# Performance work log

Measured on AMD Instinct MI355X. Metric: run time of the kernel, lower is better.

## Reference

```python
import jax, jax.numpy as jnp
import numpy as np

N = 16384   # flat token count
D = 256     # d_model
M = 64      # median_size (attention in_features / hidden_features)
OUT = 1     # output_size


def setup_inputs() -> dict:
    key = jax.random.key(0)
    ks = jax.random.split(key, 12)
    sD = 1.0 / np.sqrt(D)
    sM = 1.0 / np.sqrt(M)
    rn = lambda k, shape, s: (jax.random.normal(k, shape, jnp.float32) * s)
    return {
        "x":    rn(ks[0], (N, D), 1.0),
        "W1":   rn(ks[1], (D, M), sD), "b1": jnp.zeros((M,), jnp.float32),
        # 3 stacked attention blocks
        "Wq":   rn(ks[2], (3, M, M), sM), "bq": jnp.zeros((3, M), jnp.float32),
        "Wk":   rn(ks[3], (3, M, M), sM), "bk": jnp.zeros((3, M), jnp.float32),
        "Wv":   rn(ks[4], (3, M, M), sM), "bv": jnp.zeros((3, M), jnp.float32),
        "Wf1":  rn(ks[5], (3, M, M), sM), "bf1": jnp.zeros((3, M), jnp.float32),
        "Wf2":  rn(ks[6], (3, M, M), sM), "bf2": jnp.zeros((3, M), jnp.float32),
        "ln_g": jnp.ones((3, M), jnp.float32), "ln_b": jnp.zeros((3, M), jnp.float32),
        "Wout": rn(ks[7], (M, OUT), sM), "bout": jnp.zeros((OUT,), jnp.float32),
    }


def leaky(x, slope):
    return jnp.where(x >= 0, x, slope * x)


def layer_norm(x, g, b, eps=1e-5):
    mu = jnp.mean(x, axis=-1, keepdims=True)
    var = jnp.mean((x - mu) ** 2, axis=-1, keepdims=True)
    return (x - mu) * jax.lax.rsqrt(var + eps) * g + b


def attn_block(x, Wq, bq, Wk, bk, Wv, bv, Wf1, bf1, Wf2, bf2):
    # per-token outer-product attention: attn[n] = softmax(q[n] k[n]^T) over last dim
    q = x @ Wq + bq            # [N, M]
    k = x @ Wk + bk
    v = x @ Wv + bv
    a = jax.nn.softmax(q[:, :, None] * k[:, None, :], axis=-1)   # [N, M, M]
    y = jnp.einsum('nij,nj->ni', a, v) + x                       # residual add (x += x0)
    h = leaky(y @ Wf1 + bf1, 0.01)                               # LeakyReLU(0.01)
    h = h @ Wf2 + bf2
    return h + y                                                 # pred=False residual


def reference(x, W1, b1, Wq, bq, Wk, bk, Wv, bv, Wf1, bf1, Wf2, bf2, ln_g, ln_b, Wout, bout):
    h = x @ W1 + b1                 # Linear_1
    res = leaky(h, 0.1)             # x1 = LeakyReLU(0.1)(h)
    cur = h                         # transformer_1 is applied to pre-activation h
    for t in range(3):
        a = attn_block(cur, Wq[t], bq[t], Wk[t], bk[t], Wv[t], bv[t],
                       Wf1[t], bf1[t], Wf2[t], bf2[t])
        a = layer_norm(a, ln_g[t], ln_b[t])
        res = a + res               # x2 = LN(...) + x1, etc.
        cur = res
    out = leaky(res @ Wout + bout, 0.1).reshape(-1, OUT)
    return (out, out, out, out, out)
```

## Files before the change

kernel.cpp:

```cpp
#include <hip/hip_runtime.h>

#define NTOK 16384
#define TB 16

typedef float f32x4_t __attribute__((ext_vector_type(4)));
typedef short s16x8_t __attribute__((ext_vector_type(8)));

union bfpack { unsigned int u[4]; s16x8_t v; };

__device__ __forceinline__ unsigned int pk2bf(float lo, float hi) {
    unsigned int r;
    asm("v_cvt_pk_bf16_f32 %0, %1, %2" : "=v"(r) : "v"(lo), "v"(hi));
    return r;
}
__device__ __forceinline__ unsigned short f2bf(float f) {
    unsigned int r;
    asm("v_cvt_pk_bf16_f32 %0, %1, %1" : "=v"(r) : "v"(f));
    return (unsigned short)r;
}
__device__ __forceinline__ unsigned short f2bf_host_style(float f) {
    unsigned int x = __float_as_uint(f);
    x += 0x7fffu + ((x >> 16) & 1u);
    return (unsigned short)(x >> 16);
}
__device__ __forceinline__ float fexp2(float x) {
#if __has_builtin(__builtin_amdgcn_exp2f)
    return __builtin_amdgcn_exp2f(x);
#else
    return exp2f(x);
#endif
}
__device__ __forceinline__ float frcp(float x) {
#if __has_builtin(__builtin_amdgcn_rcpf)
    return __builtin_amdgcn_rcpf(x);
#else
    return 1.0f / x;
#endif
}
__device__ __forceinline__ float frsq(float x) {
#if __has_builtin(__builtin_amdgcn_rsqf)
    return __builtin_amdgcn_rsqf(x);
#else
    return rsqrtf(x);
#endif
}

__global__ __launch_bounds__(256)
void prep_kernel(const float* __restrict__ W1,
                 const float* __restrict__ Wq, const float* __restrict__ Wk,
                 const float* __restrict__ Wv, const float* __restrict__ Wf1,
                 const float* __restrict__ Wf2, unsigned short* __restrict__ wsb)
{
    const int i = blockIdx.x * 256 + threadIdx.x;
    if (i < 16384) {
        const int m = i >> 8, k = i & 255;
        wsb[i] = f2bf_host_style(W1[k * 64 + m]);
    } else if (i < 77824) {
        const int u  = i - 16384;
        const int mi = u >> 12;
        const int st = mi / 5, q = mi % 5;
        const int r  = u & 4095;
        const int m  = r >> 6, k = r & 63;
        const float* src = q == 0 ? Wq : q == 1 ? Wk : q == 2 ? Wv : q == 3 ? Wf1 : Wf2;
        wsb[i] = f2bf_host_style(src[st * 4096 + k * 64 + m]);
    }
}

__global__ __launch_bounds__(256, 4)
void tf3_kernel(const float* __restrict__ x,
                const float* __restrict__ b1,
                const float* __restrict__ bq, const float* __restrict__ bk,
                const float* __restrict__ bv,
                const float* __restrict__ bf1, const float* __restrict__ bf2,
                const float* __restrict__ lng, const float* __restrict__ lnb,
                const float* __restrict__ Wout, const float* __restrict__ bout,
                const unsigned short* __restrict__ wsb,
                float* __restrict__ out)
{
    __shared__ __align__(16) unsigned short w3_lds[3 * 4096];
    __shared__ __align__(16) unsigned short a_lds[16 * 64];
    __shared__ __align__(16) float q_lds[16 * 68];
    __shared__ __align__(16) float ky_lds[16 * 68];
    __shared__ __align__(16) float v_lds[16 * 68];

    const int tid = threadIdx.x;
    const int wv  = tid >> 6;
    const int l   = tid & 63;
    const int n0  = blockIdx.x * TB;

    const int lr  = l & 15;
    const int q4  = l >> 4;
    const int c   = wv * 16 + lr;

    const int ge = lr;
    const int tg = wv * 4 + q4;

    float res_reg[4], cur_reg[4];

    auto LOAD2 = [&](int matIdx, s16x8_t& r0, s16x8_t& r1) {
        const char* gb = (const char*)(wsb + 16384 + matIdx * 4096) + wv * 2048 + l * 16;
        r0 = *reinterpret_cast<const s16x8_t*>(gb);
        r1 = *reinterpret_cast<const s16x8_t*>(gb + 1024);
    };
    auto WRITE2 = [&](int slot, s16x8_t r0, s16x8_t r1) {
        #pragma unroll
        for (int p = 0; p < 2; ++p) {
            const int b  = wv * 2048 + p * 1024 + l * 16;
            const int mm = b >> 7;
            const int sw = ((b >> 4) & 7) ^ (mm & 7);
            *reinterpret_cast<s16x8_t*>((char*)w3_lds + slot * 8192 + (b & ~127) + (sw << 4))
                = p ? r1 : r0;
        }
    };
    auto mm16 = [&](s16x8_t af0, s16x8_t af1, const unsigned short* bbase) -> f32x4_t {
        const s16x8_t b0  = *reinterpret_cast<const s16x8_t*>(&bbase[c * 64 + (((0 + q4) ^ (c & 7)) * 8)]);
        const s16x8_t b1f = *reinterpret_cast<const s16x8_t*>(&bbase[c * 64 + (((4 + q4) ^ (c & 7)) * 8)]);
        f32x4_t acc = __builtin_amdgcn_mfma_f32_16x16x32_bf16(af0, b0, (f32x4_t){0.f,0.f,0.f,0.f}, 0, 0, 0);
        acc = __builtin_amdgcn_mfma_f32_16x16x32_bf16(af1, b1f, acc, 0, 0, 0);
        return acc;
    };

    s16x8_t wr0, wr1, wr2, wr3, wr4, wr5;

    LOAD2(0, wr0, wr1); LOAD2(1, wr2, wr3); LOAD2(2, wr4, wr5);

    {
        const int r  = tid & 15;
        const int cb = tid >> 4;
        const float* xp = x + (size_t)(n0 + r) * 256 + cb * 16;
        const float4 u0 = *reinterpret_cast<const float4*>(xp);
        const float4 u1 = *reinterpret_cast<const float4*>(xp + 4);
        const float4 u2 = *reinterpret_cast<const float4*>(xp + 8);
        const float4 u3 = *reinterpret_cast<const float4*>(xp + 12);
        bfpack P0, P1;
        P0.u[0] = pk2bf(u0.x, u0.y); P0.u[1] = pk2bf(u0.z, u0.w);
        P0.u[2] = pk2bf(u1.x, u1.y); P0.u[3] = pk2bf(u1.z, u1.w);
        P1.u[0] = pk2bf(u2.x, u2.y); P1.u[1] = pk2bf(u2.z, u2.w);
        P1.u[2] = pk2bf(u3.x, u3.y); P1.u[3] = pk2bf(u3.z, u3.w);
        char* rowb = (char*)w3_lds + r * 512;
        *reinterpret_cast<s16x8_t*>(rowb + (((cb * 2    ) ^ (r & 7)) << 4)) = P0.v;
        *reinterpret_cast<s16x8_t*>(rowb + (((cb * 2 + 1) ^ (r & 7)) << 4)) = P1.v;
    }
    __syncthreads();

    {
        f32x4_t acch = {0.f, 0.f, 0.f, 0.f};
        #pragma unroll
        for (int s5 = 0; s5 < 8; ++s5) {
            const s16x8_t af = *reinterpret_cast<const s16x8_t*>(
                (const char*)w3_lds + lr * 512 + ((((s5 * 4 + q4)) ^ (lr & 7)) << 4));
            const s16x8_t bf = *reinterpret_cast<const s16x8_t*>(&wsb[c * 256 + s5 * 32 + q4 * 8]);
            acch = __builtin_amdgcn_mfma_f32_16x16x32_bf16(af, bf, acch, 0, 0, 0);
        }
        const float bb = b1[c];
        #pragma unroll
        for (int rg = 0; rg < 4; ++rg)
            q_lds[(q4 * 4 + rg) * 68 + c] = acch[rg] + bb;
    }
    __syncthreads();
    WRITE2(0, wr0, wr1); WRITE2(1, wr2, wr3); WRITE2(2, wr4, wr5);
    #pragma unroll
    for (int tt = 0; tt < 4; ++tt) {
        const int t = wv * 4 + tt;
        const float h = q_lds[t * 68 + l];
        cur_reg[tt] = h;
        res_reg[tt] = h >= 0.f ? h : 0.1f * h;
        a_lds[t * 64 + (((l >> 3) ^ (t & 7)) * 8) + (l & 7)] = f2bf(h);
    }

    for (int st = 0; st < 3; ++st) {
        const float bqv  = bq[st * 64 + c];
        const float bkv  = bk[st * 64 + c];
        const float bvv  = bv[st * 64 + c];
        const float bf1v = bf1[st * 64 + c];
        const float bf2v = bf2[st * 64 + c];
        const float lngv = lng[st * 64 + l];
        const float lnbv = lnb[st * 64 + l];

        __syncthreads();
        {
            const s16x8_t af0 = *reinterpret_cast<const s16x8_t*>(&a_lds[lr * 64 + ((q4       ^ (lr & 7)) * 8)]);
            const s16x8_t af1 = *reinterpret_cast<const s16x8_t*>(&a_lds[lr * 64 + (((4 + q4) ^ (lr & 7)) * 8)]);
            f32x4_t aq = mm16(af0, af1, &w3_lds[0]);
            f32x4_t ak = mm16(af0, af1, &w3_lds[4096]);
            f32x4_t av = mm16(af0, af1, &w3_lds[8192]);
            #pragma unroll
            for (int rg = 0; rg < 4; ++rg) {
                const int tr = q4 * 4 + rg;
                q_lds[tr * 68 + c]  = aq[rg] + bqv;
                ky_lds[tr * 68 + c] = ak[rg] + bkv;
                v_lds[tr * 68 + c]  = av[rg] + bvv;
            }
        }
        LOAD2(st * 5 + 3, wr0, wr1);
        LOAD2(st * 5 + 4, wr2, wr3);
        __syncthreads();

        float kmax_t[4], kmin_t[4];
        {
            const float4 kv = *reinterpret_cast<const float4*>(&ky_lds[tg * 68 + ge * 4]);
            float kmx = fmaxf(fmaxf(kv.x, kv.y), fmaxf(kv.z, kv.w));
            float kmn = fminf(fminf(kv.x, kv.y), fminf(kv.z, kv.w));
            #pragma unroll
            for (int m = 1; m < 16; m <<= 1) {
                kmx = fmaxf(kmx, __shfl_xor(kmx, m, 64));
                kmn = fminf(kmn, __shfl_xor(kmn, m, 64));
            }
            #pragma unroll
            for (int tt = 0; tt < 4; ++tt) {
                kmax_t[tt] = __shfl(kmx, tt * 16, 64);
                kmin_t[tt] = __shfl(kmn, tt * 16, 64);
            }
        }
        #pragma unroll
        for (int tt = 0; tt < 4; ++tt) {
            const int t = wv * 4 + tt;
            const float qs = q_lds[t * 68 + l] * 1.44269504088896340736f;
            const float m2 = fmaxf(qs * kmax_t[tt], qs * kmin_t[tt]);
            const float* kb = &ky_lds[t * 68];
            const float* vb = &v_lds[t * 68];
            float4 ka0 = *reinterpret_cast<const float4*>(kb);
            float4 ka1 = *reinterpret_cast<const float4*>(kb + 4);
            float4 va0 = *reinterpret_cast<const float4*>(vb);
            float4 va1 = *reinterpret_cast<const float4*>(vb + 4);
            float s0 = 0.f, s1 = 0.f, p0 = 0.f, p1 = 0.f;
            #pragma unroll
            for (int j = 0; j < 64; j += 8) {
                float4 kn0, kn1, vn0, vn1;
                if (j < 56) {
                    kn0 = *reinterpret_cast<const float4*>(kb + j + 8);
                    kn1 = *reinterpret_cast<const float4*>(kb + j + 12);
                    vn0 = *reinterpret_cast<const float4*>(vb + j + 8);
                    vn1 = *reinterpret_cast<const float4*>(vb + j + 12);
                }
                const float e0 = fexp2(fmaf(qs, ka0.x, -m2)); s0 += e0; p0 = fmaf(e0, va0.x, p0);
                const float e1 = fexp2(fmaf(qs, ka0.y, -m2)); s1 += e1; p1 = fmaf(e1, va0.y, p1);
                const float e2 = fexp2(fmaf(qs, ka0.z, -m2)); s0 += e2; p0 = fmaf(e2, va0.z, p0);
                const float e3 = fexp2(fmaf(qs, ka0.w, -m2)); s1 += e3; p1 = fmaf(e3, va0.w, p1);
                const float e4 = fexp2(fmaf(qs, ka1.x, -m2)); s0 += e4; p0 = fmaf(e4, va1.x, p0);
                const float e5 = fexp2(fmaf(qs, ka1.y, -m2)); s1 += e5; p1 = fmaf(e5, va1.y, p1);
                const float e6 = fexp2(fmaf(qs, ka1.z, -m2)); s0 += e6; p0 = fmaf(e6, va1.z, p0);
                const float e7 = fexp2(fmaf(qs, ka1.w, -m2)); s1 += e7; p1 = fmaf(e7, va1.w, p1);
                ka0 = kn0; ka1 = kn1; va0 = vn0; va1 = vn1;
            }
            const float y = (p0 + p1) * frcp(s0 + s1) + cur_reg[tt];
            ky_lds[t * 68 + l] = y;
        }
        __syncthreads();

        WRITE2(0, wr0, wr1); WRITE2(1, wr2, wr3);

        {
            f32x4_t acc = {0.f, 0.f, 0.f, 0.f};
            #pragma unroll
            for (int kh = 0; kh < 2; ++kh) {
                const float* yp = &ky_lds[lr * 68 + kh * 32 + q4 * 8];
                const float4 y0 = *reinterpret_cast<const float4*>(yp);
                const float4 y1 = *reinterpret_cast<const float4*>(yp + 4);
                bfpack P;
                P.u[0] = pk2bf(y0.x, y0.y); P.u[1] = pk2bf(y0.z, y0.w);
                P.u[2] = pk2bf(y1.x, y1.y); P.u[3] = pk2bf(y1.z, y1.w);
                const int ck = kh * 4 + q4;
                const s16x8_t bf = *reinterpret_cast<const s16x8_t*>(&w3_lds[c * 64 + ((ck ^ (c & 7)) * 8)]);
                acc = __builtin_amdgcn_mfma_f32_16x16x32_bf16(P.v, bf, acc, 0, 0, 0);
            }
            #pragma unroll
            for (int rg = 0; rg < 4; ++rg) {
                const int tr = q4 * 4 + rg;
                float h = acc[rg] + bf1v;
                h = h >= 0.f ? h : 0.01f * h;
                a_lds[tr * 64 + (((c >> 3) ^ (tr & 7)) * 8) + (c & 7)] = f2bf(h);
            }
        }
        if (st < 2) {
            LOAD2((st + 1) * 5 + 0, wr0, wr1);
            LOAD2((st + 1) * 5 + 1, wr2, wr3);
            LOAD2((st + 1) * 5 + 2, wr4, wr5);
        }
        __syncthreads();

        {
            const s16x8_t ag0 = *reinterpret_cast<const s16x8_t*>(&a_lds[lr * 64 + ((q4       ^ (lr & 7)) * 8)]);
            const s16x8_t ag1 = *reinterpret_cast<const s16x8_t*>(&a_lds[lr * 64 + (((4 + q4) ^ (lr & 7)) * 8)]);
            f32x4_t acc = mm16(ag0, ag1, &w3_lds[4096]);
            #pragma unroll
            for (int rg = 0; rg < 4; ++rg) {
                const int tr = q4 * 4 + rg;
                ky_lds[tr * 68 + c] += acc[rg] + bf2v;
            }
        }
        __syncthreads();

        {
            const float4 av4 = *reinterpret_cast<const float4*>(&ky_lds[tg * 68 + ge * 4]);
            float ssum = av4.x + av4.y + av4.z + av4.w;
            #pragma unroll
            for (int m = 1; m < 16; m <<= 1) ssum += __shfl_xor(ssum, m, 64);
            const float mug = ssum * 0.015625f;
            const float d0 = av4.x - mug, d1 = av4.y - mug, d2 = av4.z - mug, d3 = av4.w - mug;
            float vsum = d0 * d0 + d1 * d1 + d2 * d2 + d3 * d3;
            #pragma unroll
            for (int m = 1; m < 16; m <<= 1) vsum += __shfl_xor(vsum, m, 64);
            #pragma unroll
            for (int tt = 0; tt < 4; ++tt) {
                const int t = wv * 4 + tt;
                const float mu = __shfl(mug, tt * 16, 64);
                const float vv = __shfl(vsum, tt * 16, 64);
                const float rs = frsq(vv * 0.015625f + 1e-5f);
                const float a  = ky_lds[t * 68 + l];
                const float an = (a - mu) * rs * lngv + lnbv;
                const float rnew = res_reg[tt] + an;
                res_reg[tt] = rnew;
                cur_reg[tt] = rnew;
                a_lds[t * 64 + (((l >> 3) ^ (t & 7)) * 8) + (l & 7)] = f2bf(rnew);
            }
        }
        if (st < 2) { WRITE2(0, wr0, wr1); WRITE2(1, wr2, wr3); WRITE2(2, wr4, wr5); }
    }

    const float wo = Wout[l];
    const float bo = bout[0];
    #pragma unroll
    for (int tt = 0; tt < 4; ++tt)
        q_lds[(wv * 4 + tt) * 68 + l] = res_reg[tt] * wo;
    {
        const float4 pv = *reinterpret_cast<const float4*>(&q_lds[tg * 68 + ge * 4]);
        float p = pv.x + pv.y + pv.z + pv.w;
        #pragma unroll
        for (int m = 1; m < 16; m <<= 1) p += __shfl_xor(p, m, 64);
        if (ge == 0) {
            float o = p + bo;
            o = o >= 0.f ? o : 0.1f * o;
            #pragma unroll
            for (int c5 = 0; c5 < 5; ++c5)
                out[(size_t)c5 * NTOK + n0 + tg] = o;
        }
    }
}

extern "C" void kernel_launch(void* const* d_in, const int* in_sizes, int n_in,
                              void* d_out, int out_size, void* d_ws, size_t ws_size,
                              hipStream_t stream) {
    const float* x    = (const float*)d_in[0];
    const float* W1   = (const float*)d_in[1];
    const float* b1   = (const float*)d_in[2];
    const float* Wq   = (const float*)d_in[3];
    const float* bq   = (const float*)d_in[4];
    const float* Wk   = (const float*)d_in[5];
    const float* bk   = (const float*)d_in[6];
    const float* Wv   = (const float*)d_in[7];
    const float* bv   = (const float*)d_in[8];
    const float* Wf1  = (const float*)d_in[9];
    const float* bf1  = (const float*)d_in[10];
    const float* Wf2  = (const float*)d_in[11];
    const float* bf2  = (const float*)d_in[12];
    const float* lngp = (const float*)d_in[13];
    const float* lnbp = (const float*)d_in[14];
    const float* Wout = (const float*)d_in[15];
    const float* bout = (const float*)d_in[16];
    float* outp = (float*)d_out;
    unsigned short* wsb = (unsigned short*)d_ws;

    hipLaunchKernelGGL(prep_kernel, dim3(304), dim3(256), 0, stream,
                       W1, Wq, Wk, Wv, Wf1, Wf2, wsb);
    hipLaunchKernelGGL(tf3_kernel, dim3(NTOK / TB), dim3(256), 0, stream,
                       x, b1, bq, bk, bv, bf1, bf2, lngp, lnbp, Wout, bout,
                       (const unsigned short*)wsb, outp);
}
```

Measured before the change: 57.40 us.

## Load weight MFMA fragments directly from global into registers, drop LDS weight staging

The prep kernel now writes the per-stage weight matrices in a layout that matches the MFMA B-fragment, so each lane loads its operands straight from global memory into registers. The 24KB LDS weight buffer and its swizzled writes are removed, and the x staging image is aliased onto the q/ky/v buffers, shrinking LDS to about 15KB. Launch bounds are raised to target 5 blocks per CU. The cost is extra register pressure and global/L2 load latency that is now exposed inside the stage loop, with loads issued one phase ahead of use.

```diff
diff --git a/kernel.cpp b/kernel.cpp
--- a/kernel.cpp
+++ b/kernel.cpp
@@ -60,13 +60,20 @@
         const int mi = u >> 12;
         const int st = mi / 5, q = mi % 5;
         const int r  = u & 4095;
-        const int m  = r >> 6, k = r & 63;
+        const int hk = r >> 11;
+        const int r1 = r & 2047;
+        const int w  = r1 >> 9;
+        const int r2 = r1 & 511;
+        const int l  = r2 >> 3;
+        const int e  = r2 & 7;
+        const int m  = w * 16 + (l & 15);
+        const int k  = hk * 32 + (l >> 4) * 8 + e;
         const float* src = q == 0 ? Wq : q == 1 ? Wk : q == 2 ? Wv : q == 3 ? Wf1 : Wf2;
         wsb[i] = f2bf_host_style(src[st * 4096 + k * 64 + m]);
     }
 }
 
-__global__ __launch_bounds__(256, 4)
+__global__ __launch_bounds__(256, 5)
 void tf3_kernel(const float* __restrict__ x,
                 const float* __restrict__ b1,
                 const float* __restrict__ bq, const float* __restrict__ bk,
@@ -77,11 +84,12 @@
                 const unsigned short* __restrict__ wsb,
                 float* __restrict__ out)
 {
-    __shared__ __align__(16) unsigned short w3_lds[3 * 4096];
-    __shared__ __align__(16) unsigned short a_lds[16 * 64];
-    __shared__ __align__(16) float q_lds[16 * 68];
-    __shared__ __align__(16) float ky_lds[16 * 68];
-    __shared__ __align__(16) float v_lds[16 * 68];
+    __shared__ __align__(16) char smem[15104];
+    unsigned short* a_lds = (unsigned short*)smem;
+    float* q_lds  = (float*)(smem + 2048);
+    float* ky_lds = (float*)(smem + 6400);
+    float* v_lds  = (float*)(smem + 10752);
+    char*  x_img  = smem + 2048;
 
     const int tid = threadIdx.x;
     const int wv  = tid >> 6;
@@ -97,32 +105,21 @@
 
     float res_reg[4], cur_reg[4];
 
-    auto LOAD2 = [&](int matIdx, s16x8_t& r0, s16x8_t& r1) {
-        const char* gb = (const char*)(wsb + 16384 + matIdx * 4096) + wv * 2048 + l * 16;
+    auto LOADM = [&](int mat, s16x8_t& r0, s16x8_t& r1) {
+        const char* gb = (const char*)(wsb + 16384 + mat * 4096) + wv * 1024 + l * 16;
         r0 = *reinterpret_cast<const s16x8_t*>(gb);
-        r1 = *reinterpret_cast<const s16x8_t*>(gb + 1024);
+        r1 = *reinterpret_cast<const s16x8_t*>(gb + 4096);
     };
-    auto WRITE2 = [&](int slot, s16x8_t r0, s16x8_t r1) {
-        #pragma unroll
-        for (int p = 0; p < 2; ++p) {
-            const int b  = wv * 2048 + p * 1024 + l * 16;
-            const int mm = b >> 7;
-            const int sw = ((b >> 4) & 7) ^ (mm & 7);
-            *reinterpret_cast<s16x8_t*>((char*)w3_lds + slot * 8192 + (b & ~127) + (sw << 4))
-                = p ? r1 : r0;
-        }
-    };
-    auto mm16 = [&](s16x8_t af0, s16x8_t af1, const unsigned short* bbase) -> f32x4_t {
-        const s16x8_t b0  = *reinterpret_cast<const s16x8_t*>(&bbase[c * 64 + (((0 + q4) ^ (c & 7)) * 8)]);
-        const s16x8_t b1f = *reinterpret_cast<const s16x8_t*>(&bbase[c * 64 + (((4 + q4) ^ (c & 7)) * 8)]);
+    auto mmd = [&](s16x8_t af0, s16x8_t af1, s16x8_t b0, s16x8_t b1) -> f32x4_t {
         f32x4_t acc = __builtin_amdgcn_mfma_f32_16x16x32_bf16(af0, b0, (f32x4_t){0.f,0.f,0.f,0.f}, 0, 0, 0);
-        acc = __builtin_amdgcn_mfma_f32_16x16x32_bf16(af1, b1f, acc, 0, 0, 0);
+        acc = __builtin_amdgcn_mfma_f32_16x16x32_bf16(af1, b1, acc, 0, 0, 0);
         return acc;
     };
 
-    s16x8_t wr0, wr1, wr2, wr3, wr4, wr5;
-
-    LOAD2(0, wr0, wr1); LOAD2(1, wr2, wr3); LOAD2(2, wr4, wr5);
+    s16x8_t bq0, bq1, bk0, bk1, bv0, bv1;
+    s16x8_t f10, f11, f20, f21;
+
+    LOADM(0, bq0, bq1); LOADM(1, bk0, bk1); LOADM(2, bv0, bv1);
 
     {
         const int r  = tid & 15;
@@ -137,28 +134,28 @@
         P0.u[2] = pk2bf(u1.x, u1.y); P0.u[3] = pk2bf(u1.z, u1.w);
         P1.u[0] = pk2bf(u2.x, u2.y); P1.u[1] = pk2bf(u2.z, u2.w);
         P1.u[2] = pk2bf(u3.x, u3.y); P1.u[3] = pk2bf(u3.z, u3.w);
-        char* rowb = (char*)w3_lds + r * 512;
+        char* rowb = x_img + r * 512;
         *reinterpret_cast<s16x8_t*>(rowb + (((cb * 2    ) ^ (r & 7)) << 4)) = P0.v;
         *reinterpret_cast<s16x8_t*>(rowb + (((cb * 2 + 1) ^ (r & 7)) << 4)) = P1.v;
     }
     __syncthreads();
 
+    f32x4_t acch = {0.f, 0.f, 0.f, 0.f};
+    #pragma unroll
+    for (int s5 = 0; s5 < 8; ++s5) {
+        const s16x8_t af = *reinterpret_cast<const s16x8_t*>(
+            x_img + lr * 512 + (((s5 * 4 + q4) ^ (lr & 7)) << 4));
+        const s16x8_t bf = *reinterpret_cast<const s16x8_t*>(&wsb[c * 256 + s5 * 32 + q4 * 8]);
+        acch = __builtin_amdgcn_mfma_f32_16x16x32_bf16(af, bf, acch, 0, 0, 0);
+    }
+    __syncthreads();
     {
-        f32x4_t acch = {0.f, 0.f, 0.f, 0.f};
-        #pragma unroll
-        for (int s5 = 0; s5 < 8; ++s5) {
-            const s16x8_t af = *reinterpret_cast<const s16x8_t*>(
-                (const char*)w3_lds + lr * 512 + ((((s5 * 4 + q4)) ^ (lr & 7)) << 4));
-            const s16x8_t bf = *reinterpret_cast<const s16x8_t*>(&wsb[c * 256 + s5 * 32 + q4 * 8]);
-            acch = __builtin_amdgcn_mfma_f32_16x16x32_bf16(af, bf, acch, 0, 0, 0);
-        }
         const float bb = b1[c];
         #pragma unroll
         for (int rg = 0; rg < 4; ++rg)
             q_lds[(q4 * 4 + rg) * 68 + c] = acch[rg] + bb;
     }
     __syncthreads();
-    WRITE2(0, wr0, wr1); WRITE2(1, wr2, wr3); WRITE2(2, wr4, wr5);
     #pragma unroll
     for (int tt = 0; tt < 4; ++tt) {
         const int t = wv * 4 + tt;
@@ -181,9 +178,9 @@
         {
             const s16x8_t af0 = *reinterpret_cast<const s16x8_t*>(&a_lds[lr * 64 + ((q4       ^ (lr & 7)) * 8)]);
             const s16x8_t af1 = *reinterpret_cast<const s16x8_t*>(&a_lds[lr * 64 + (((4 + q4) ^ (lr & 7)) * 8)]);
-            f32x4_t aq = mm16(af0, af1, &w3_lds[0]);
-            f32x4_t ak = mm16(af0, af1, &w3_lds[4096]);
-            f32x4_t av = mm16(af0, af1, &w3_lds[8192]);
+            f32x4_t aq = mmd(af0, af1, bq0, bq1);
+            f32x4_t ak = mmd(af0, af1, bk0, bk1);
+            f32x4_t av = mmd(af0, af1, bv0, bv1);
             #pragma unroll
             for (int rg = 0; rg < 4; ++rg) {
                 const int tr = q4 * 4 + rg;
@@ -192,8 +189,7 @@
                 v_lds[tr * 68 + c]  = av[rg] + bvv;
             }
         }
-        LOAD2(st * 5 + 3, wr0, wr1);
-        LOAD2(st * 5 + 4, wr2, wr3);
+        LOADM(st * 5 + 3, f10, f11);
         __syncthreads();
 
         float kmax_t[4], kmin_t[4];
@@ -246,9 +242,8 @@
             const float y = (p0 + p1) * frcp(s0 + s1) + cur_reg[tt];
             ky_lds[t * 68 + l] = y;
         }
-        __syncthreads();
-
-        WRITE2(0, wr0, wr1); WRITE2(1, wr2, wr3);
+        LOADM(st * 5 + 4, f20, f21);
+        __syncthreads();
 
         {
             f32x4_t acc = {0.f, 0.f, 0.f, 0.f};
@@ -260,9 +255,7 @@
                 bfpack P;
                 P.u[0] = pk2bf(y0.x, y0.y); P.u[1] = pk2bf(y0.z, y0.w);
                 P.u[2] = pk2bf(y1.x, y1.y); P.u[3] = pk2bf(y1.z, y1.w);
-                const int ck = kh * 4 + q4;
-                const s16x8_t bf = *reinterpret_cast<const s16x8_t*>(&w3_lds[c * 64 + ((ck ^ (c & 7)) * 8)]);
-                acc = __builtin_amdgcn_mfma_f32_16x16x32_bf16(P.v, bf, acc, 0, 0, 0);
+                acc = __builtin_amdgcn_mfma_f32_16x16x32_bf16(P.v, kh ? f11 : f10, acc, 0, 0, 0);
             }
             #pragma unroll
             for (int rg = 0; rg < 4; ++rg) {
@@ -273,22 +266,22 @@
             }
         }
         if (st < 2) {
-            LOAD2((st + 1) * 5 + 0, wr0, wr1);
-            LOAD2((st + 1) * 5 + 1, wr2, wr3);
-            LOAD2((st + 1) * 5 + 2, wr4, wr5);
+            LOADM((st + 1) * 5 + 0, bq0, bq1);
+            LOADM((st + 1) * 5 + 1, bk0, bk1);
         }
         __syncthreads();
 
         {
             const s16x8_t ag0 = *reinterpret_cast<const s16x8_t*>(&a_lds[lr * 64 + ((q4       ^ (lr & 7)) * 8)]);
             const s16x8_t ag1 = *reinterpret_cast<const s16x8_t*>(&a_lds[lr * 64 + (((4 + q4) ^ (lr & 7)) * 8)]);
-            f32x4_t acc = mm16(ag0, ag1, &w3_lds[4096]);
+            f32x4_t acc = mmd(ag0, ag1, f20, f21);
             #pragma unroll
             for (int rg = 0; rg < 4; ++rg) {
                 const int tr = q4 * 4 + rg;
                 ky_lds[tr * 68 + c] += acc[rg] + bf2v;
             }
         }
+        if (st < 2) LOADM((st + 1) * 5 + 2, bv0, bv1);
         __syncthreads();
 
         {
@@ -315,7 +308,6 @@
                 a_lds[t * 64 + (((l >> 3) ^ (t & 7)) * 8) + (l & 7)] = f2bf(rnew);
             }
         }
-        if (st < 2) { WRITE2(0, wr0, wr1); WRITE2(1, wr2, wr3); WRITE2(2, wr4, wr5); }
     }
 
     const float wo = Wout[l];
```

Result: slower. 80.33 us (+39.9%).
